# Performance work log

Measured on AMD Instinct MI355X. Metric: run time of the kernel, lower is better.

The kernel has to match this reference:

```python
import jax, jax.numpy as jnp
import numpy as np

N, E, IN, C, H = 50000, 800000, 128, 64, 4

def setup_inputs() -> dict:
    key = jax.random.key(0)
    ks = jax.random.split(key, 32)
    rn = lambda k, s, sc=0.05: (jax.random.normal(k, s, dtype=jnp.float32) * sc)
    inp = {
        'x': rn(ks[0], (N, IN), 1.0),
        'edge_index': jax.random.randint(ks[1], (2, E), 0, N, dtype=jnp.int32),
        # GATConv 1: 128 -> 4 heads x 64, concat
        'W1': rn(ks[2], (IN, H * C)), 'as1': rn(ks[3], (H, C)), 'ad1': rn(ks[4], (H, C)), 'bias1': jnp.zeros((H * C,), jnp.float32),
        'g1': jnp.ones((H * C,), jnp.float32), 'be1': jnp.zeros((H * C,), jnp.float32),
        # GATConv 2: 256 -> 4 heads x 64, concat
        'W2': rn(ks[5], (H * C, H * C)), 'as2': rn(ks[6], (H, C)), 'ad2': rn(ks[7], (H, C)), 'bias2': jnp.zeros((H * C,), jnp.float32),
        'g2': jnp.ones((H * C,), jnp.float32), 'be2': jnp.zeros((H * C,), jnp.float32),
        # GATConv 3: 256 -> 1 head x 32, no concat
        'W3': rn(ks[8], (H * C, 32)), 'as3': rn(ks[9], (1, 32)), 'ad3': rn(ks[10], (1, 32)), 'bias3': jnp.zeros((32,), jnp.float32),
        'g3': jnp.ones((32,), jnp.float32), 'be3': jnp.zeros((32,), jnp.float32),
        # classifier 32 -> 32 -> 1
        'Wc1': rn(ks[11], (32, 32), 0.2), 'bc1': jnp.zeros((32,), jnp.float32),
        'Wc2': rn(ks[12], (32, 1), 0.2), 'bc2': jnp.zeros((1,), jnp.float32),
    }
    return inp


def _gat(x, src, dst, W, a_s, a_d, b, heads, out_c, concat, n_nodes):
    # linear transform + head split: [N, heads, out_c]
    h = (x @ W).reshape(-1, heads, out_c)
    # per-node attention logits, gathered onto edges
    al_s = (h * a_s).sum(-1)  # [N, heads]
    al_d = (h * a_d).sum(-1)
    e = jax.nn.leaky_relu(al_s[src] + al_d[dst], 0.2)  # [E, heads]
    # segment softmax over incoming edges of each target node
    m = jax.ops.segment_max(e, dst, num_segments=n_nodes)
    ex = jnp.exp(e - m[dst])
    denom = jax.ops.segment_sum(ex, dst, num_segments=n_nodes)
    alpha = ex / (denom[dst] + 1e-16)
    # weighted message scatter-add
    out = jax.ops.segment_sum(h[src] * alpha[:, :, None], dst, num_segments=n_nodes)
    out = out.reshape(n_nodes, heads * out_c) if concat else out.mean(axis=1)
    return out + b


def _bn(x, g, be):
    mu = x.mean(0)
    var = x.var(0)
    return (x - mu) * jax.lax.rsqrt(var + 1e-5) * g + be


def reference(x, edge_index, W1, as1, ad1, bias1, g1, be1, W2, as2, ad2, bias2, g2, be2,
              W3, as3, ad3, bias3, g3, be3, Wc1, bc1, Wc2, bc2):
    n = x.shape[0]
    loop = jnp.arange(n, dtype=edge_index.dtype)  # PyG GATConv adds self-loops
    src = jnp.concatenate([edge_index[0], loop])
    dst = jnp.concatenate([edge_index[1], loop])
    x = jax.nn.elu(_bn(_gat(x, src, dst, W1, as1, ad1, bias1, H, C, True, n), g1, be1))
    x = jax.nn.elu(_bn(_gat(x, src, dst, W2, as2, ad2, bias2, H, C, True, n), g2, be2))
    x = jax.nn.elu(_bn(_gat(x, src, dst, W3, as3, ad3, bias3, 1, 32, False, n), g3, be3))
    hcls = jax.nn.relu(x @ Wc1 + bc1)
    return (hcls @ Wc2 + bc2).squeeze(-1)  # [N]
```

## Files before the change

### kernel.cpp

```cpp
#include <hip/hip_runtime.h>
#include <math.h>

typedef __attribute__((ext_vector_type(8))) short short8;
typedef __attribute__((ext_vector_type(4))) float f32x4;


__device__ __forceinline__ float bf2f(unsigned short u) {
  union { unsigned int i; float f; } v;
  v.i = ((unsigned int)u) << 16;
  return v.f;
}
__device__ __forceinline__ unsigned short f2bf(float f) {
  union { float f; unsigned int i; } v;
  v.f = f;
  unsigned int x = v.i;
  unsigned int r = x + 0x7fffu + ((x >> 16) & 1u);
  return (unsigned short)(r >> 16);
}
__device__ __forceinline__ float lo16f(unsigned int u) {
  union { unsigned int i; float f; } v;
  v.i = u << 16;
  return v.f;
}
__device__ __forceinline__ float hi16f(unsigned int u) {
  union { unsigned int i; float f; } v;
  v.i = u & 0xffff0000u;
  return v.f;
}


__global__ __launch_bounds__(256) void count_deg(const int* __restrict__ dstA,
                                                 int Ee, int Nn,
                                                 int* __restrict__ deg) {
  int e = blockIdx.x * 256 + threadIdx.x;
  if (e >= Ee + Nn) return;
  int d = (e < Ee) ? dstA[e] : (e - Ee);
  atomicAdd(&deg[d], 1);
}

__global__ __launch_bounds__(256) void scan_blk(const int* __restrict__ deg,
                                                int* __restrict__ exc,
                                                int* __restrict__ bsum, int Nn) {
  __shared__ int sd[256];
  int t = threadIdx.x;
  int i = blockIdx.x * 256 + t;
  int v = (i < Nn) ? deg[i] : 0;
  sd[t] = v;
  __syncthreads();
  #pragma unroll
  for (int s = 1; s < 256; s <<= 1) {
    int u = (t >= s) ? sd[t - s] : 0;
    __syncthreads();
    sd[t] += u;
    __syncthreads();
  }
  if (i < Nn) exc[i] = sd[t] - v;
  if (t == 255) bsum[blockIdx.x] = sd[255];
}

__global__ void scan_top(const int* __restrict__ bsum, int* __restrict__ boff,
                         int NB, int* __restrict__ off, int Nn) {
  __shared__ int sd[256];
  int t = threadIdx.x;
  int v = (t < NB) ? bsum[t] : 0;
  sd[t] = v;
  __syncthreads();
  #pragma unroll
  for (int s = 1; s < 256; s <<= 1) {
    int u = (t >= s) ? sd[t - s] : 0;
    __syncthreads();
    sd[t] += u;
    __syncthreads();
  }
  if (t < NB) boff[t] = sd[t] - v;
  if (t == 255) off[Nn] = sd[255];
}

__global__ __launch_bounds__(256) void scan_add(const int* __restrict__ exc,
                                                const int* __restrict__ boff,
                                                int* __restrict__ off,
                                                int* __restrict__ cursor, int Nn) {
  int i = blockIdx.x * 256 + threadIdx.x;
  if (i >= Nn) return;
  int o = exc[i] + boff[blockIdx.x];
  off[i] = o;
  cursor[i] = o;
}

__global__ __launch_bounds__(256) void fill_csr(const int* __restrict__ srcA,
                                                const int* __restrict__ dstA,
                                                int Ee, int Nn,
                                                int* __restrict__ cursor,
                                                int* __restrict__ col) {
  int e = blockIdx.x * 256 + threadIdx.x;
  if (e >= Ee + Nn) return;
  int s, d;
  if (e < Ee) { s = srcA[e]; d = dstA[e]; }
  else        { s = e - Ee;  d = s; }
  int slot = atomicAdd(&cursor[d], 1);
  col[slot] = s;
}


__global__ __launch_bounds__(256) void cast_f32_bf16(const float* __restrict__ in,
                                                     unsigned short* __restrict__ out,
                                                     size_t n4) {
  for (size_t i = blockIdx.x * (size_t)256 + threadIdx.x; i < n4;
       i += (size_t)gridDim.x * 256) {
    float4 v = *(const float4*)&in[i * 4];
    ushort4 o;
    o.x = f2bf(v.x); o.y = f2bf(v.y); o.z = f2bf(v.z); o.w = f2bf(v.w);
    *(ushort4*)&out[i * 4] = o;
  }
}

__global__ __launch_bounds__(256) void transpose_cast(const float* __restrict__ W,
                                                      unsigned short* __restrict__ Wt,
                                                      int K, int N) {
  int t = blockIdx.x * 256 + threadIdx.x;
  if (t >= K * N) return;
  int n = t / K, k = t % K;
  Wt[t] = f2bf(W[(size_t)k * N + n]);
}


template <int BM, int BN, int WM, int WN, int HEADS, int CC>
__global__ __launch_bounds__(256) void gemm_mfma_logits(
    const unsigned short* __restrict__ A,
    const unsigned short* __restrict__ Bt,
    unsigned short* __restrict__ C,
    const float* __restrict__ a_s, const float* __restrict__ a_d,
    float* __restrict__ als, float* __restrict__ ald,
    int M, int N, int K) {
  static_assert(WN == CC, "wave col-range must equal head width");
  constexpr int BK = 32;
  constexpr int LDA = BK + 8;
  constexpr int MF = WM / 16, NF = WN / 16;
  constexpr int NWN = BN / WN;
  constexpr int ACH = BM * BK / 8;
  constexpr int BCH = BN * BK / 8;
  constexpr int ACHT = (ACH + 255) / 256;
  constexpr int BCHT = (BCH + 255) / 256;

  __shared__ unsigned short Al[2][BM * LDA];
  __shared__ unsigned short Bl[2][BN * LDA];

  const int tid = threadIdx.x;
  const int wid = tid >> 6, lane = tid & 63;
  const int wr = wid / NWN, wc = wid % NWN;
  const int brow = blockIdx.y * BM;
  const int bcol = blockIdx.x * BN;

  f32x4 acc[MF][NF] = {};
  uint4 ra[ACHT], rb[BCHT];

  auto loadG = [&](int k0) {
    #pragma unroll
    for (int c = 0; c < ACHT; ++c) {
      int i = c * 256 + tid;
      if (ACH % 256 == 0 || i < ACH) {
        int row = i >> 2, blk = i & 3;
        int rg = brow + row;
        rg = rg < M ? rg : M - 1;
        ra[c] = *(const uint4*)&A[(size_t)rg * K + k0 + blk * 8];
      }
    }
    #pragma unroll
    for (int c = 0; c < BCHT; ++c) {
      int i = c * 256 + tid;
      if (BCH % 256 == 0 || i < BCH) {
        int row = i >> 2, blk = i & 3;
        rb[c] = *(const uint4*)&Bt[(size_t)(bcol + row) * K + k0 + blk * 8];
      }
    }
  };
  auto storeL = [&](int buf) {
    #pragma unroll
    for (int c = 0; c < ACHT; ++c) {
      int i = c * 256 + tid;
      if (ACH % 256 == 0 || i < ACH) {
        int row = i >> 2, blk = i & 3;
        *(uint4*)&Al[buf][row * LDA + blk * 8] = ra[c];
      }
    }
    #pragma unroll
    for (int c = 0; c < BCHT; ++c) {
      int i = c * 256 + tid;
      if (BCH % 256 == 0 || i < BCH) {
        int row = i >> 2, blk = i & 3;
        *(uint4*)&Bl[buf][row * LDA + blk * 8] = rb[c];
      }
    }
  };

  const int nt = K / BK;
  loadG(0);
  storeL(0);
  __syncthreads();
  int cur = 0;
  const int arow = wr * WM + (lane & 15);
  const int bro = wc * WN + (lane & 15);
  const int kb = (lane >> 4) * 8;
  for (int t = 0; t < nt; ++t) {
    if (t + 1 < nt) loadG((t + 1) * BK);
    short8 af[MF], bfr[NF];
    #pragma unroll
    for (int m = 0; m < MF; ++m)
      af[m] = *(const short8*)&Al[cur][(arow + m * 16) * LDA + kb];
    #pragma unroll
    for (int n = 0; n < NF; ++n)
      bfr[n] = *(const short8*)&Bl[cur][(bro + n * 16) * LDA + kb];
    #pragma unroll
    for (int m = 0; m < MF; ++m)
      #pragma unroll
      for (int n = 0; n < NF; ++n)
        acc[m][n] = __builtin_amdgcn_mfma_f32_16x16x32_bf16(af[m], bfr[n], acc[m][n], 0, 0, 0);
    if (t + 1 < nt) storeL(cur ^ 1);
    __syncthreads();
    cur ^= 1;
  }

  const int crow0 = brow + wr * WM + (lane >> 4) * 4;
  const int ccol0 = bcol + wc * WN + (lane & 15);
  #pragma unroll
  for (int m = 0; m < MF; ++m) {
    #pragma unroll
    for (int r = 0; r < 4; ++r) {
      int grow = crow0 + m * 16 + r;
      if (grow >= M) continue;
      #pragma unroll
      for (int n = 0; n < NF; ++n)
        C[(size_t)grow * N + ccol0 + n * 16] = f2bf(acc[m][n][r]);
    }
  }

  const int hidx = (bcol + wc * WN) / CC;
  float asv[NF], adv[NF];
  #pragma unroll
  for (int n = 0; n < NF; ++n) {
    int ch = (lane & 15) + n * 16;
    asv[n] = a_s[hidx * CC + ch];
    adv[n] = a_d[hidx * CC + ch];
  }
  #pragma unroll
  for (int m = 0; m < MF; ++m) {
    #pragma unroll
    for (int r = 0; r < 4; ++r) {
      float ps = 0.f, pd = 0.f;
      #pragma unroll
      for (int n = 0; n < NF; ++n) {
        float v = acc[m][n][r];
        ps += v * asv[n];
        pd += v * adv[n];
      }
      #pragma unroll
      for (int o = 1; o < 16; o <<= 1) {
        ps += __shfl_xor(ps, o, 64);
        pd += __shfl_xor(pd, o, 64);
      }
      int grow = crow0 + m * 16 + r;
      if ((lane & 15) == 0 && grow < M) {
        als[(size_t)grow * HEADS + hidx] = ps;
        ald[(size_t)grow * HEADS + hidx] = pd;
      }
    }
  }
}


template <int HEADS, int CC>
__global__ __launch_bounds__(256) void gat_aggregate(const unsigned short* __restrict__ h,
                                                     const float* __restrict__ als,
                                                     const float* __restrict__ ald,
                                                     const int* __restrict__ off,
                                                     const int* __restrict__ col,
                                                     const float* __restrict__ bias,
                                                     unsigned short* __restrict__ out,
                                                     int Nn) {
  constexpr int HC = HEADS * CC;
  int wid = (int)((blockIdx.x * (size_t)blockDim.x + threadIdx.x) >> 6);
  int lane = threadIdx.x & 63;
  if (wid >= Nn) return;
  int c0 = lane * 4;
  int head = c0 / CC;
  float my_ald = ald[(size_t)wid * HEADS + head];
  float ssum = 0.f;
  float acc[4] = {};
  int beg = off[wid], end = off[wid + 1];

  auto lrelu = [](float l) { return (l > 0.f) ? l : 0.2f * l; };

  int j = beg;
  for (; j + 8 <= end; j += 8) {
    int sI[8];
    ushort4 g[8];
    float p[8];
    #pragma unroll
    for (int k = 0; k < 8; ++k) sI[k] = col[j + k];
    #pragma unroll
    for (int k = 0; k < 8; ++k)
      g[k] = *(const ushort4*)(h + (size_t)sI[k] * HC + c0);
    #pragma unroll
    for (int k = 0; k < 8; ++k)
      p[k] = __expf(lrelu(als[(size_t)sI[k] * HEADS + head] + my_ald));
    #pragma unroll
    for (int k = 0; k < 8; ++k) {
      ssum += p[k];
      acc[0] += p[k] * bf2f(g[k].x);
      acc[1] += p[k] * bf2f(g[k].y);
      acc[2] += p[k] * bf2f(g[k].z);
      acc[3] += p[k] * bf2f(g[k].w);
    }
  }
  for (; j + 4 <= end; j += 4) {
    int sI[4];
    ushort4 g[4];
    float p[4];
    #pragma unroll
    for (int k = 0; k < 4; ++k) sI[k] = col[j + k];
    #pragma unroll
    for (int k = 0; k < 4; ++k)
      g[k] = *(const ushort4*)(h + (size_t)sI[k] * HC + c0);
    #pragma unroll
    for (int k = 0; k < 4; ++k)
      p[k] = __expf(lrelu(als[(size_t)sI[k] * HEADS + head] + my_ald));
    #pragma unroll
    for (int k = 0; k < 4; ++k) {
      ssum += p[k];
      acc[0] += p[k] * bf2f(g[k].x);
      acc[1] += p[k] * bf2f(g[k].y);
      acc[2] += p[k] * bf2f(g[k].z);
      acc[3] += p[k] * bf2f(g[k].w);
    }
  }
  for (; j < end; ++j) {
    int s = col[j];
    float p = __expf(lrelu(als[(size_t)s * HEADS + head] + my_ald));
    ssum += p;
    ushort4 hv = *(const ushort4*)(h + (size_t)s * HC + c0);
    acc[0] += p * bf2f(hv.x);
    acc[1] += p * bf2f(hv.y);
    acc[2] += p * bf2f(hv.z);
    acc[3] += p * bf2f(hv.w);
  }
  float inv = 1.f / (ssum + 1e-16f);
  #pragma unroll
  for (int k2 = 0; k2 < 4; ++k2)
    out[(size_t)wid * HC + c0 + k2] = f2bf(acc[k2] * inv + bias[c0 + k2]);
}


template <int CC>
__global__ __launch_bounds__(256) void gat_aggregate_splitk(
    const unsigned short* __restrict__ h, const float* __restrict__ als,
    const float* __restrict__ ald, const int* __restrict__ off,
    const int* __restrict__ col, const float* __restrict__ bias,
    unsigned short* __restrict__ out, int Nn) {
  int wid = (int)((blockIdx.x * (size_t)blockDim.x + threadIdx.x) >> 6);
  int lane = threadIdx.x & 63;
  if (wid >= Nn) return;
  int c = lane & (CC - 1);
  int half = lane >> 5;
  float my_ald = ald[wid];
  int beg0 = off[wid], end0 = off[wid + 1];
  int mid = beg0 + ((end0 - beg0) >> 1);
  int beg = half ? mid : beg0;
  int end = half ? end0 : mid;

  auto lrelu = [](float l) { return (l > 0.f) ? l : 0.2f * l; };

  float ssum = 0.f, acc = 0.f;
  int j = beg;
  for (; j + 4 <= end; j += 4) {
    int s0 = col[j], s1 = col[j + 1], s2 = col[j + 2], s3 = col[j + 3];
    unsigned short g0 = h[(size_t)s0 * CC + c];
    unsigned short g1 = h[(size_t)s1 * CC + c];
    unsigned short g2 = h[(size_t)s2 * CC + c];
    unsigned short g3 = h[(size_t)s3 * CC + c];
    float p0 = __expf(lrelu(als[s0] + my_ald));
    float p1 = __expf(lrelu(als[s1] + my_ald));
    float p2 = __expf(lrelu(als[s2] + my_ald));
    float p3 = __expf(lrelu(als[s3] + my_ald));
    ssum += (p0 + p1) + (p2 + p3);
    acc += p0 * bf2f(g0) + p1 * bf2f(g1) + p2 * bf2f(g2) + p3 * bf2f(g3);
  }
  for (; j < end; ++j) {
    int s = col[j];
    float p = __expf(lrelu(als[s] + my_ald));
    ssum += p;
    acc += p * bf2f(h[(size_t)s * CC + c]);
  }
  ssum += __shfl_xor(ssum, 32, 64);
  acc += __shfl_xor(acc, 32, 64);
  if (half == 0)
    out[(size_t)wid * CC + c] = f2bf(acc / (ssum + 1e-16f) + bias[c]);
}


constexpr int BN_NB = 1024;

template <int CH>
__global__ __launch_bounds__(256) void bn_stats_part(const unsigned short* __restrict__ x,
                                                     int Nn, float* __restrict__ pbuf) {
  constexpr int Q8 = CH / 8;
  int t = threadIdx.x;
  size_t tot8 = (size_t)Nn * Q8;
  size_t stride = (size_t)gridDim.x * 256;
  float s[8] = {}, sq[8] = {};
  for (size_t i = blockIdx.x * (size_t)256 + t; i < tot8; i += stride) {
    uint4 u = *(const uint4*)&x[i * 8];
    float v[8] = {lo16f(u.x), hi16f(u.x), lo16f(u.y), hi16f(u.y),
                  lo16f(u.z), hi16f(u.z), lo16f(u.w), hi16f(u.w)};
    #pragma unroll
    for (int k = 0; k < 8; ++k) { s[k] += v[k]; sq[k] += v[k] * v[k]; }
  }
  __shared__ float sS[256][8];
  __shared__ float sQ[256][8];
  #pragma unroll
  for (int k = 0; k < 8; ++k) { sS[t][k] = s[k]; sQ[t][k] = sq[k]; }
  __syncthreads();
  for (int half = 128; half >= Q8; half >>= 1) {
    if (t < half) {
      #pragma unroll
      for (int k = 0; k < 8; ++k) {
        sS[t][k] += sS[t + half][k];
        sQ[t][k] += sQ[t + half][k];
      }
    }
    __syncthreads();
  }
  if (t < Q8) {
    #pragma unroll
    for (int k = 0; k < 8; ++k) {
      pbuf[(size_t)blockIdx.x * 2 * CH + t * 8 + k] = sS[t][k];
      pbuf[(size_t)blockIdx.x * 2 * CH + CH + t * 8 + k] = sQ[t][k];
    }
  }
}

template <int CH>
__global__ __launch_bounds__(256) void bn_reduce_finalize(const float* __restrict__ pbuf,
                                                          const float* __restrict__ g,
                                                          const float* __restrict__ be,
                                                          float invN,
                                                          float* __restrict__ ss) {
  int c = blockIdx.x;
  int t = threadIdx.x;
  float s = 0.f, q = 0.f;
  for (int b = t; b < BN_NB; b += 256) {
    s += pbuf[(size_t)b * 2 * CH + c];
    q += pbuf[(size_t)b * 2 * CH + CH + c];
  }
  #pragma unroll
  for (int o = 32; o > 0; o >>= 1) {
    s += __shfl_xor(s, o, 64);
    q += __shfl_xor(q, o, 64);
  }
  __shared__ float rs[4], rq[4];
  int wv = t >> 6, lane = t & 63;
  if (lane == 0) { rs[wv] = s; rq[wv] = q; }
  __syncthreads();
  if (t == 0) {
    float S = rs[0] + rs[1] + rs[2] + rs[3];
    float Qs = rq[0] + rq[1] + rq[2] + rq[3];
    float mu = S * invN;
    float var = Qs * invN - mu * mu;
    float sc = g[c] * rsqrtf(var + 1e-5f);
    ss[c] = sc;
    ss[CH + c] = be[c] - mu * sc;
  }
}

template <int CH>
__global__ __launch_bounds__(256) void bn_apply_elu_b2b(const unsigned short* __restrict__ x,
                                                        const float* __restrict__ ss,
                                                        unsigned short* __restrict__ out,
                                                        int Nn) {
  size_t tot8 = (size_t)Nn * (CH / 8);
  for (size_t i = blockIdx.x * (size_t)256 + threadIdx.x; i < tot8;
       i += (size_t)gridDim.x * 256) {
    uint4 u = *(const uint4*)&x[i * 8];
    int c0 = (int)((i % (CH / 8)) * 8);
    float v[8] = {lo16f(u.x), hi16f(u.x), lo16f(u.y), hi16f(u.y),
                  lo16f(u.z), hi16f(u.z), lo16f(u.w), hi16f(u.w)};
    unsigned int o[4];
    #pragma unroll
    for (int k = 0; k < 4; ++k) {
      float y0 = v[2 * k] * ss[c0 + 2 * k] + ss[CH + c0 + 2 * k];
      float y1 = v[2 * k + 1] * ss[c0 + 2 * k + 1] + ss[CH + c0 + 2 * k + 1];
      y0 = (y0 > 0.f) ? y0 : expm1f(y0);
      y1 = (y1 > 0.f) ? y1 : expm1f(y1);
      o[k] = (unsigned int)f2bf(y0) | ((unsigned int)f2bf(y1) << 16);
    }
    *(uint4*)&out[i * 8] = make_uint4(o[0], o[1], o[2], o[3]);
  }
}


__global__ __launch_bounds__(256) void classifier_k(const unsigned short* __restrict__ x,
                                                    const float* __restrict__ Wc1,
                                                    const float* __restrict__ bc1,
                                                    const float* __restrict__ Wc2,
                                                    const float* __restrict__ bc2,
                                                    float* __restrict__ outp, int Nn) {
  __shared__ unsigned short sx[256][33];
  __shared__ float sw[32 * 32];
  __shared__ float sb1[32];
  __shared__ float sw2[32];
  int t = threadIdx.x;
  int base = blockIdx.x * 256;
  for (int i = t; i < 1024; i += 256) sw[i] = Wc1[i];
  if (t < 32) { sb1[t] = bc1[t]; sw2[t] = Wc2[t]; }
  int cnt = min(256, Nn - base);
  for (int i = t; i < cnt * 32; i += 256) sx[i / 32][i % 32] = x[(size_t)base * 32 + i];
  __syncthreads();
  if (t < cnt) {
    float xa[32];
    #pragma unroll
    for (int c = 0; c < 32; ++c) xa[c] = bf2f(sx[t][c]);
    float o = bc2[0];
    #pragma unroll
    for (int j = 0; j < 32; ++j) {
      float v = sb1[j];
      #pragma unroll
      for (int c = 0; c < 32; ++c) v += xa[c] * sw[c * 32 + j];
      v = fmaxf(v, 0.f);
      o += v * sw2[j];
    }
    outp[base + t] = o;
  }
}


extern "C" void kernel_launch(void* const* d_in, const int* in_sizes, int n_in,
                              void* d_out, int out_size, void* d_ws, size_t ws_size,
                              hipStream_t stream) {
  const float* x   = (const float*)d_in[0];
  const int*   ei  = (const int*)d_in[1];
  const float* W1  = (const float*)d_in[2];
  const float* as1 = (const float*)d_in[3];
  const float* ad1 = (const float*)d_in[4];
  const float* b1  = (const float*)d_in[5];
  const float* g1  = (const float*)d_in[6];
  const float* be1 = (const float*)d_in[7];
  const float* W2  = (const float*)d_in[8];
  const float* as2 = (const float*)d_in[9];
  const float* ad2 = (const float*)d_in[10];
  const float* b2  = (const float*)d_in[11];
  const float* g2  = (const float*)d_in[12];
  const float* be2 = (const float*)d_in[13];
  const float* W3  = (const float*)d_in[14];
  const float* as3 = (const float*)d_in[15];
  const float* ad3 = (const float*)d_in[16];
  const float* b3  = (const float*)d_in[17];
  const float* g3  = (const float*)d_in[18];
  const float* be3 = (const float*)d_in[19];
  const float* Wc1 = (const float*)d_in[20];
  const float* bc1 = (const float*)d_in[21];
  const float* Wc2 = (const float*)d_in[22];
  const float* bc2 = (const float*)d_in[23];
  float* outp = (float*)d_out;

  const int Nn = in_sizes[0] / 128;
  const int Ee = in_sizes[1] / 2;
  const int TotE = Ee + Nn;
  const int* esrc = ei;
  const int* edst = ei + Ee;

  char* w = (char*)d_ws;
  auto carve = [&](size_t bytes) {
    char* p = w;
    w += (bytes + 255) & ~(size_t)255;
    return p;
  };
  unsigned short* hb  = (unsigned short*)carve((size_t)Nn * 256 * 2);
  unsigned short* xb  = (unsigned short*)carve((size_t)Nn * 256 * 2);
  unsigned short* agg = (unsigned short*)carve((size_t)Nn * 256 * 2);
  float* als   = (float*)carve((size_t)Nn * 4 * 4);
  float* ald   = (float*)carve((size_t)Nn * 4 * 4);
  float* pbuf  = (float*)carve((size_t)BN_NB * 512 * 4);
  float* ss    = (float*)carve(512 * 4);
  unsigned short* Wt1 = (unsigned short*)carve(256 * 128 * 2);
  unsigned short* Wt2 = (unsigned short*)carve(256 * 256 * 2);
  unsigned short* Wt3 = (unsigned short*)carve(32 * 256 * 2);
  int* deg     = (int*)carve((size_t)Nn * 4);
  int* off     = (int*)carve((size_t)(Nn + 1) * 4);
  int* cursor  = (int*)carve((size_t)Nn * 4);
  int* col     = (int*)carve((size_t)TotE * 4);
  int* exc     = (int*)carve((size_t)Nn * 4);
  int* bsum    = (int*)carve(256 * 4);
  int* boff    = (int*)carve(256 * 4);

  cast_f32_bf16<<<2048, 256, 0, stream>>>(x, xb, (size_t)Nn * 128 / 4);
  transpose_cast<<<(128 * 256 + 255) / 256, 256, 0, stream>>>(W1, Wt1, 128, 256);
  transpose_cast<<<(256 * 256 + 255) / 256, 256, 0, stream>>>(W2, Wt2, 256, 256);
  transpose_cast<<<(256 * 32 + 255) / 256, 256, 0, stream>>>(W3, Wt3, 256, 32);

  const int NB = (Nn + 255) / 256;
  hipMemsetAsync(deg, 0, (size_t)Nn * 4, stream);
  count_deg<<<(TotE + 255) / 256, 256, 0, stream>>>(edst, Ee, Nn, deg);
  scan_blk<<<NB, 256, 0, stream>>>(deg, exc, bsum, Nn);
  scan_top<<<1, 256, 0, stream>>>(bsum, boff, NB, off, Nn);
  scan_add<<<NB, 256, 0, stream>>>(exc, boff, off, cursor, Nn);
  fill_csr<<<(TotE + 255) / 256, 256, 0, stream>>>(esrc, edst, Ee, Nn, cursor, col);

  int waveBlocks = (Nn + 3) / 4;
  int gy = (Nn + 127) / 128;
  float invN = 1.0f / (float)Nn;

  gemm_mfma_logits<128, 128, 64, 64, 4, 64><<<dim3(2, gy), 256, 0, stream>>>(
      xb, Wt1, hb, as1, ad1, als, ald, Nn, 256, 128);
  gat_aggregate<4, 64><<<waveBlocks, 256, 0, stream>>>(hb, als, ald, off, col, b1, agg, Nn);
  bn_stats_part<256><<<BN_NB, 256, 0, stream>>>(agg, Nn, pbuf);
  bn_reduce_finalize<256><<<256, 256, 0, stream>>>(pbuf, g1, be1, invN, ss);
  bn_apply_elu_b2b<256><<<2048, 256, 0, stream>>>(agg, ss, xb, Nn);

  gemm_mfma_logits<128, 128, 64, 64, 4, 64><<<dim3(2, gy), 256, 0, stream>>>(
      xb, Wt2, hb, as2, ad2, als, ald, Nn, 256, 256);
  gat_aggregate<4, 64><<<waveBlocks, 256, 0, stream>>>(hb, als, ald, off, col, b2, agg, Nn);
  bn_stats_part<256><<<BN_NB, 256, 0, stream>>>(agg, Nn, pbuf);
  bn_reduce_finalize<256><<<256, 256, 0, stream>>>(pbuf, g2, be2, invN, ss);
  bn_apply_elu_b2b<256><<<2048, 256, 0, stream>>>(agg, ss, xb, Nn);

  gemm_mfma_logits<128, 32, 32, 32, 1, 32><<<dim3(1, gy), 256, 0, stream>>>(
      xb, Wt3, hb, as3, ad3, als, ald, Nn, 32, 256);
  gat_aggregate_splitk<32><<<waveBlocks, 256, 0, stream>>>(hb, als, ald, off, col, b3, agg, Nn);
  bn_stats_part<32><<<BN_NB, 256, 0, stream>>>(agg, Nn, pbuf);
  bn_reduce_finalize<32><<<32, 256, 0, stream>>>(pbuf, g3, be3, invN, ss);
  bn_apply_elu_b2b<32><<<512, 256, 0, stream>>>(agg, ss, agg, Nn);

  classifier_k<<<(Nn + 255) / 256, 256, 0, stream>>>(agg, Wc1, bc1, Wc2, bc2, outp, Nn);
}
```

Measured before the change: 435.6 us.

## Build CSR via two-level bucket sort with shared-memory atomics

Replaces the global-atomic degree count, three-kernel scan and global-atomic fill with a two-pass bucket sort. Edges are first histogrammed and scattered into 128-node buckets using per-block shared-memory counters, then each bucket is locally sorted into CSR with shared-memory atomics. This removes heavy contention on global atomics and the random writes to col. In exchange it adds an intermediate 8-byte-per-edge buffer and an extra pass over the edges, and node count is capped at MAXBUK*128.

```diff
diff --git a/kernel.cpp b/kernel.cpp
--- a/kernel.cpp
+++ b/kernel.cpp
@@ -29,22 +29,35 @@
 }
 
 
-__global__ __launch_bounds__(256) void count_deg(const int* __restrict__ dstA,
-                                                 int Ee, int Nn,
-                                                 int* __restrict__ deg) {
-  int e = blockIdx.x * 256 + threadIdx.x;
-  if (e >= Ee + Nn) return;
-  int d = (e < Ee) ? dstA[e] : (e - Ee);
-  atomicAdd(&deg[d], 1);
-}
-
-__global__ __launch_bounds__(256) void scan_blk(const int* __restrict__ deg,
-                                                int* __restrict__ exc,
-                                                int* __restrict__ bsum, int Nn) {
+constexpr int CSR_HB = 256;
+constexpr int BUK_SH = 7;
+constexpr int MAXBUK = 512;
+
+__global__ __launch_bounds__(256) void bucket_hist(const int* __restrict__ dstA,
+                                                   int Ee, int Nn, int nbuk,
+                                                   int* __restrict__ bhist) {
+  __shared__ int hist[MAXBUK];
+  int t = threadIdx.x;
+  for (int i = t; i < nbuk; i += 256) hist[i] = 0;
+  __syncthreads();
+  int TotE = Ee + Nn;
+  int chunk = (TotE + CSR_HB - 1) / CSR_HB;
+  int base = blockIdx.x * chunk;
+  int lim = min(base + chunk, TotE);
+  for (int e = base + t; e < lim; e += 256) {
+    int d = (e < Ee) ? dstA[e] : (e - Ee);
+    atomicAdd(&hist[d >> BUK_SH], 1);
+  }
+  __syncthreads();
+  for (int i = t; i < nbuk; i += 256)
+    bhist[(size_t)i * CSR_HB + blockIdx.x] = hist[i];
+}
+
+__global__ __launch_bounds__(256) void bucket_scan(int* __restrict__ bhist,
+                                                   int* __restrict__ btot) {
   __shared__ int sd[256];
-  int t = threadIdx.x;
-  int i = blockIdx.x * 256 + t;
-  int v = (i < Nn) ? deg[i] : 0;
+  int b = blockIdx.x, t = threadIdx.x;
+  int v = bhist[(size_t)b * CSR_HB + t];
   sd[t] = v;
   __syncthreads();
   #pragma unroll
@@ -54,51 +67,92 @@
     sd[t] += u;
     __syncthreads();
   }
-  if (i < Nn) exc[i] = sd[t] - v;
-  if (t == 255) bsum[blockIdx.x] = sd[255];
-}
-
-__global__ void scan_top(const int* __restrict__ bsum, int* __restrict__ boff,
-                         int NB, int* __restrict__ off, int Nn) {
-  __shared__ int sd[256];
+  bhist[(size_t)b * CSR_HB + t] = sd[t] - v;
+  if (t == 255) btot[b] = sd[255];
+}
+
+__global__ __launch_bounds__(MAXBUK) void bucket_base(const int* __restrict__ btot,
+                                                      int* __restrict__ bucketBase,
+                                                      int nbuk) {
+  __shared__ int sd[MAXBUK];
   int t = threadIdx.x;
-  int v = (t < NB) ? bsum[t] : 0;
+  int v = (t < nbuk) ? btot[t] : 0;
   sd[t] = v;
   __syncthreads();
   #pragma unroll
-  for (int s = 1; s < 256; s <<= 1) {
+  for (int s = 1; s < MAXBUK; s <<= 1) {
     int u = (t >= s) ? sd[t - s] : 0;
     __syncthreads();
     sd[t] += u;
     __syncthreads();
   }
-  if (t < NB) boff[t] = sd[t] - v;
-  if (t == 255) off[Nn] = sd[255];
-}
-
-__global__ __launch_bounds__(256) void scan_add(const int* __restrict__ exc,
-                                                const int* __restrict__ boff,
-                                                int* __restrict__ off,
-                                                int* __restrict__ cursor, int Nn) {
-  int i = blockIdx.x * 256 + threadIdx.x;
-  if (i >= Nn) return;
-  int o = exc[i] + boff[blockIdx.x];
-  off[i] = o;
-  cursor[i] = o;
-}
-
-__global__ __launch_bounds__(256) void fill_csr(const int* __restrict__ srcA,
-                                                const int* __restrict__ dstA,
-                                                int Ee, int Nn,
-                                                int* __restrict__ cursor,
-                                                int* __restrict__ col) {
-  int e = blockIdx.x * 256 + threadIdx.x;
-  if (e >= Ee + Nn) return;
-  int s, d;
-  if (e < Ee) { s = srcA[e]; d = dstA[e]; }
-  else        { s = e - Ee;  d = s; }
-  int slot = atomicAdd(&cursor[d], 1);
-  col[slot] = s;
+  if (t < nbuk) bucketBase[t] = sd[t] - v;
+  if (t == nbuk - 1) bucketBase[nbuk] = sd[t];
+}
+
+__global__ __launch_bounds__(256) void bucket_scatter(const int* __restrict__ srcA,
+                                                      const int* __restrict__ dstA,
+                                                      int Ee, int Nn, int nbuk,
+                                                      const int* __restrict__ bhist,
+                                                      const int* __restrict__ bucketBase,
+                                                      int2* __restrict__ ebuf) {
+  __shared__ int cursor[MAXBUK];
+  int t = threadIdx.x;
+  for (int i = t; i < nbuk; i += 256)
+    cursor[i] = bhist[(size_t)i * CSR_HB + blockIdx.x] + bucketBase[i];
+  __syncthreads();
+  int TotE = Ee + Nn;
+  int chunk = (TotE + CSR_HB - 1) / CSR_HB;
+  int base = blockIdx.x * chunk;
+  int lim = min(base + chunk, TotE);
+  for (int e = base + t; e < lim; e += 256) {
+    int s, d;
+    if (e < Ee) { s = srcA[e]; d = dstA[e]; }
+    else        { s = e - Ee;  d = s; }
+    int slot = atomicAdd(&cursor[d >> BUK_SH], 1);
+    ebuf[slot] = make_int2(s, d);
+  }
+}
+
+__global__ __launch_bounds__(256) void fine_fill(const int2* __restrict__ ebuf,
+                                                 const int* __restrict__ bucketBase,
+                                                 int Nn, int TotE,
+                                                 int* __restrict__ off,
+                                                 int* __restrict__ col) {
+  __shared__ int ndeg[128];
+  __shared__ int ncur[128];
+  __shared__ int sd[128];
+  int b = blockIdx.x, t = threadIdx.x;
+  int n0 = b << BUK_SH;
+  int ncnt = min(128, Nn - n0);
+  int ebeg = bucketBase[b], eend = bucketBase[b + 1];
+  if (t < 128) ndeg[t] = 0;
+  __syncthreads();
+  for (int e = ebeg + t; e < eend; e += 256)
+    atomicAdd(&ndeg[ebuf[e].y - n0], 1);
+  __syncthreads();
+  if (t < 128) sd[t] = ndeg[t];
+  __syncthreads();
+  #pragma unroll
+  for (int s = 1; s < 128; s <<= 1) {
+    int u = 0;
+    if (t < 128 && t >= s) u = sd[t - s];
+    __syncthreads();
+    if (t < 128) sd[t] += u;
+    __syncthreads();
+  }
+  if (t < 128) {
+    int base = ebeg + sd[t] - ndeg[t];
+    ncur[t] = base;
+    if (t < ncnt) off[n0 + t] = base;
+  }
+  if (b == 0 && t == 0) off[Nn] = TotE;
+  __syncthreads();
+  for (int e = ebeg + t; e < eend; e += 256) {
+    int2 ed = ebuf[e];
+    int slot = atomicAdd(&ncur[ed.y - n0], 1);
+    col[slot] = ed.x;
+  }
 }
 
 
@@ -583,26 +637,24 @@
   unsigned short* Wt1 = (unsigned short*)carve(256 * 128 * 2);
   unsigned short* Wt2 = (unsigned short*)carve(256 * 256 * 2);
   unsigned short* Wt3 = (unsigned short*)carve(32 * 256 * 2);
-  int* deg     = (int*)carve((size_t)Nn * 4);
   int* off     = (int*)carve((size_t)(Nn + 1) * 4);
-  int* cursor  = (int*)carve((size_t)Nn * 4);
   int* col     = (int*)carve((size_t)TotE * 4);
-  int* exc     = (int*)carve((size_t)Nn * 4);
-  int* bsum    = (int*)carve(256 * 4);
-  int* boff    = (int*)carve(256 * 4);
+  int2* ebuf   = (int2*)carve((size_t)TotE * 8);
+  int* bhist   = (int*)carve((size_t)MAXBUK * CSR_HB * 4);
+  int* btot    = (int*)carve(MAXBUK * 4);
+  int* bucketBase = (int*)carve((MAXBUK + 1) * 4);
 
   cast_f32_bf16<<<2048, 256, 0, stream>>>(x, xb, (size_t)Nn * 128 / 4);
   transpose_cast<<<(128 * 256 + 255) / 256, 256, 0, stream>>>(W1, Wt1, 128, 256);
   transpose_cast<<<(256 * 256 + 255) / 256, 256, 0, stream>>>(W2, Wt2, 256, 256);
   transpose_cast<<<(256 * 32 + 255) / 256, 256, 0, stream>>>(W3, Wt3, 256, 32);
 
-  const int NB = (Nn + 255) / 256;
-  hipMemsetAsync(deg, 0, (size_t)Nn * 4, stream);
-  count_deg<<<(TotE + 255) / 256, 256, 0, stream>>>(edst, Ee, Nn, deg);
-  scan_blk<<<NB, 256, 0, stream>>>(deg, exc, bsum, Nn);
-  scan_top<<<1, 256, 0, stream>>>(bsum, boff, NB, off, Nn);
-  scan_add<<<NB, 256, 0, stream>>>(exc, boff, off, cursor, Nn);
-  fill_csr<<<(TotE + 255) / 256, 256, 0, stream>>>(esrc, edst, Ee, Nn, cursor, col);
+  const int nbuk = (Nn + 127) >> BUK_SH;
+  bucket_hist<<<CSR_HB, 256, 0, stream>>>(edst, Ee, Nn, nbuk, bhist);
+  bucket_scan<<<nbuk, 256, 0, stream>>>(bhist, btot);
+  bucket_base<<<1, MAXBUK, 0, stream>>>(btot, bucketBase, nbuk);
+  bucket_scatter<<<CSR_HB, 256, 0, stream>>>(esrc, edst, Ee, Nn, nbuk, bhist, bucketBase, ebuf);
+  fine_fill<<<nbuk, 256, 0, stream>>>(ebuf, bucketBase, Nn, TotE, off, col);
 
   int waveBlocks = (Nn + 3) / 4;
   int gy = (Nn + 127) / 128;
```

Measured after the change: 360.7 us. 1.21x faster.
